# Optimization experiments

Measured on AMD Instinct MI355X. Metric: run time of the kernel, lower is better.

The kernel has to match this reference:

```python
import jax, jax.numpy as jnp
import numpy as np

NSTEP, NGRID, MU = 730, 2000, 16
PRECS = 1e-5

# HBV parameter scaling ranges (parascaLst)
_LO = np.array([1, 50, 0.05, 0.01, 0.001, 0.2, 0, 0, -2.5, 0.5, 0, 0, 0.3], dtype=np.float32)
_HI = np.array([6, 1000, 0.9, 0.5, 0.2, 1, 10, 100, 2.5, 10, 0.1, 0.2, 5], dtype=np.float32)


def setup_inputs() -> dict:
    key = jax.random.key(0)
    k1, k2 = jax.random.split(key)
    u = jax.random.uniform(k1, (NSTEP, NGRID, 3), dtype=jnp.float32)
    # channel 0: precip [0,10]; channel 1: temp [-5,15]; channel 2: PET [0,5]
    scale = jnp.array([10.0, 20.0, 5.0], dtype=jnp.float32)
    shift = jnp.array([0.0, -5.0, 0.0], dtype=jnp.float32)
    x = u * scale + shift
    parameters = jax.random.uniform(k2, (NGRID, 13, MU), dtype=jnp.float32)
    return {"x": x, "parameters": parameters, "mu": MU}


def _hbv_forward(x, parameters, mu):
    Ngrid = x.shape[1]
    lo = jnp.asarray(_LO)[None, :, None]
    hi = jnp.asarray(_HI)[None, :, None]
    p = lo + parameters * (hi - lo)  # [Ngrid, 13, mu]
    (parBETA, parFC, parK0, parK1, parK2, parLP, parPERC, parUZL,
     parTT, parCFMAX, parCFR, parCWH, parBETAET) = [p[:, i, :] for i in range(13)]

    init = jnp.full((Ngrid, mu), 0.001, dtype=jnp.float32)
    state0 = (init, init, init, init, init)  # SNOWPACK, MELTWATER, SM, SUZ, SLZ

    def step(carry, inp):
        SP, MW, SM, SUZ, SLZ = carry
        Pt, Tt, Et = inp  # each [Ngrid]
        Pt, Tt, Et = Pt[:, None], Tt[:, None], Et[:, None]  # broadcast over mu
        rain = Pt * (Tt >= parTT).astype(jnp.float32)
        snow = Pt * (Tt < parTT).astype(jnp.float32)
        SP = SP + snow
        melt = jnp.minimum(jnp.maximum(parCFMAX * (Tt - parTT), 0.0), SP)
        MW = MW + melt
        SP = SP - melt
        refreezing = jnp.minimum(jnp.maximum(parCFR * parCFMAX * (parTT - Tt), 0.0), MW)
        SP = SP + refreezing
        MW = MW - refreezing
        tosoil = jnp.maximum(MW - parCWH * SP, 0.0)
        MW = MW - tosoil
        soil_wetness = jnp.clip((SM / parFC) ** parBETA, 0.0, 1.0)
        recharge = (rain + tosoil) * soil_wetness
        SM = SM + rain + tosoil - recharge
        excess = jnp.maximum(SM - parFC, 0.0)
        SM = SM - excess
        evapfactor = jnp.clip((SM / (parLP * parFC)) ** parBETAET, 0.0, 1.0)
        ETact = jnp.minimum(SM, Et * evapfactor)
        SM = jnp.maximum(SM - ETact, PRECS)
        SUZ = SUZ + recharge + excess
        PERC = jnp.minimum(SUZ, parPERC)
        SUZ = SUZ - PERC
        Q0 = parK0 * jnp.maximum(SUZ - parUZL, 0.0)
        SUZ = SUZ - Q0
        Q1 = parK1 * SUZ
        SUZ = SUZ - Q1
        SLZ = SLZ + PERC
        Q2 = parK2 * SLZ
        SLZ = SLZ - Q2
        return (SP, MW, SM, SUZ, SLZ), Q0 + Q1 + Q2

    xs = (x[:, :, 0], x[:, :, 1], x[:, :, 2])
    _, Qsimmu = jax.lax.scan(step, state0, xs)  # [Nstep, Ngrid, mu]
    Qsimave = Qsimmu.mean(-1)  # muwts=None -> mean over components
    return Qsimave[..., None]  # [Nstep, Ngrid, 1]  (routOpt=False)


def reference(x, parameters, mu):
    return _hbv_forward(x, parameters, mu)
```

## Files before the change

### kernel.cpp

```cpp
#include <hip/hip_runtime.h>

#define NSTEP  730
#define NGRID  2000
#define PRECSf 1e-5f

#define GLOBAL_AS __attribute__((address_space(1)))
#define LDS_AS    __attribute__((address_space(3)))

__device__ __forceinline__ float fast_exp2(float v) { return __builtin_amdgcn_exp2f(v); }
__device__ __forceinline__ float fast_log2(float v) { return __builtin_amdgcn_logf(v); }
__device__ __forceinline__ float med3(float a, float b, float c) {
    return __builtin_amdgcn_fmed3f(a, b, c);
}

struct Par {
    float TT, cfmax, cfmaxTT, cfrXcf, cfrTT, CWH;
    float beta, betaC, FC, betaet, betaetC;
    float PERC, omK0, k0uzl, omK1, K2;
};

#define MEMFENCE() asm volatile("" ::: "memory")
#define WAITV(N)  asm volatile("s_waitcnt vmcnt(" #N ")" ::: "memory")

__device__ __forceinline__ float route_step(float infl,
        float& SUZ, float& SLZ, const Par& c)
{
    const float SUZ1  = SUZ + infl;
    const float PERCv = fminf(SUZ1, c.PERC);
    const float SUZ2  = SUZ1 - PERCv;
    const float SUZ3  = fminf(SUZ2, fmaf(c.omK0, SUZ2, c.k0uzl));
    const float SUZ4  = c.omK1 * SUZ3;
    SUZ = SUZ4;
    const float SLZ1 = SLZ + PERCv;
    const float Q2   = c.K2 * SLZ1;
    SLZ = SLZ1 - Q2;
    return (SUZ2 - SUZ4) + Q2;
}

template<int I, bool SNOW>
__device__ __forceinline__ void step1(const float4 (&xv)[16],
        const float (&A)[16], const float (&Ets)[16],
        float (&An)[16], float (&Etn)[16],
        float (&qbuf)[16], float& infl,
        float& SM, float& SUZ, float& SLZ,
        float& SP, float& MW, const Par& c)
{
    const float Ac   = A[I];
    const float Et   = Ets[I];
    const float SMpA = SM + Ac;
    const float lg   = fast_log2(SM);
    float rain = 0.0f, SP2v = 0.0f, MW1v = 0.0f, rrawv = 0.0f, Ex = 0.0f;
    if constexpr (SNOW) {
        const float Pt = xv[I].x, Tt = xv[I].y;
        Ex = xv[I].z;
        const float snow = (Tt < c.TT) ? Pt : 0.0f;
        rain = Pt - snow;
        const float mraw = fmaf(c.cfmax, Tt, -c.cfmaxTT);
        rrawv = fmaf(-c.cfrXcf, Tt, c.cfrTT);
        const float SP1 = SP + snow;
        SP2v = med3(SP1 - mraw, 0.0f, SP1);
        MW1v = MW + (SP1 - SP2v);
    }
    const float sw = fast_exp2(fmaf(c.beta, lg, c.betaC));
    if constexpr (I >= 1) qbuf[I - 1] = route_step(infl, SUZ, SLZ, c);
    const float SM1 = fmaf(-Ac, sw, SMpA);
    const float lg1 = fast_log2(SM1);
    if constexpr (SNOW) {
        const float MW2 = med3(MW1v - rrawv, 0.0f, MW1v);
        SP = SP2v + (MW1v - MW2);
        const float tosoil = fmaxf(fmaf(-c.CWH, SP, MW2), 0.0f);
        MW = MW2 - tosoil;
        An[I]  = rain + tosoil;
        Etn[I] = Ex;
    }
    const float SM2 = fminf(SM1, c.FC);
    infl = SMpA - SM2;
    const float Ete = Et * fast_exp2(fmaf(c.betaet, lg1, c.betaetC));
    SM = fmaxf(fmaxf(SM2 - Ete, SM2 - Et), PRECSf);
}

template<int I, int NS, bool SNOW>
__device__ __forceinline__ void steps_pass(const float4 (&xv)[16],
        const float (&A)[16], const float (&Ets)[16],
        float (&An)[16], float (&Etn)[16],
        float (&qbuf)[16], float& infl,
        float& SM, float& SUZ, float& SLZ,
        float& SP, float& MW, const Par& c)
{
    if constexpr (I < NS) {
        step1<I, SNOW>(xv, A, Ets, An, Etn, qbuf, infl, SM, SUZ, SLZ, SP, MW, c);
        steps_pass<I + 1, NS, SNOW>(xv, A, Ets, An, Etn, qbuf, infl,
                                    SM, SUZ, SLZ, SP, MW, c);
    }
}

template<int I, int NS>
__device__ __forceinline__ void snow_pass(const float4 (&xv)[16],
        float& SP, float& MW, float (&A)[16], float (&Ets)[16], const Par& c)
{
    if constexpr (I < NS) {
        const float Pt = xv[I].x, Tt = xv[I].y, Ex = xv[I].z;
        const float snow = (Tt < c.TT) ? Pt : 0.0f;
        const float rain = Pt - snow;
        const float mraw = fmaf(c.cfmax, Tt, -c.cfmaxTT);
        const float rraw = fmaf(-c.cfrXcf, Tt, c.cfrTT);
        const float SP1  = SP + snow;
        const float SP2  = med3(SP1 - mraw, 0.0f, SP1);
        const float MW1  = MW + (SP1 - SP2);
        const float MW2  = med3(MW1 - rraw, 0.0f, MW1);
        SP = SP2 + (MW1 - MW2);
        const float tosoil = fmaxf(fmaf(-c.CWH, SP, MW2), 0.0f);
        MW = MW2 - tosoil;
        A[I]   = rain + tosoil;
        Ets[I] = Ex;
        snow_pass<I + 1, NS>(xv, SP, MW, A, Ets, c);
    }
}

#define LOAD_XV(B)                                                             \
    _Pragma("unroll")                                                          \
    for (int ii = 0; ii < 16; ++ii)                                            \
        xv[ii] = *reinterpret_cast<const float4*>(&xs[B][ii * 16 + crow * 4]); \
    asm volatile("" :: "v"(xv[0].x),  "v"(xv[1].x),  "v"(xv[2].x),             \
                       "v"(xv[3].x),  "v"(xv[4].x),  "v"(xv[5].x),             \
                       "v"(xv[6].x),  "v"(xv[7].x),  "v"(xv[8].x),             \
                       "v"(xv[9].x),  "v"(xv[10].x), "v"(xv[11].x),            \
                       "v"(xv[12].x), "v"(xv[13].x), "v"(xv[14].x),            \
                       "v"(xv[15].x))

#define REDUCE_STORE(T0, N) do {                                               \
    float* qrow = &qt[crow * 336 + m * 20];                                    \
    *reinterpret_cast<float4*>(qrow + 0)  = make_float4(qbuf[0], qbuf[1], qbuf[2], qbuf[3]);    \
    *reinterpret_cast<float4*>(qrow + 4)  = make_float4(qbuf[4], qbuf[5], qbuf[6], qbuf[7]);    \
    *reinterpret_cast<float4*>(qrow + 8)  = make_float4(qbuf[8], qbuf[9], qbuf[10], qbuf[11]);  \
    *reinterpret_cast<float4*>(qrow + 12) = make_float4(qbuf[12], qbuf[13], qbuf[14], qbuf[15]);\
    const float* qcol = &qt[crow * 336 + m];                                   \
    float s0 = qcol[0*20]  + qcol[1*20];                                       \
    float s1 = qcol[2*20]  + qcol[3*20];                                       \
    float s2 = qcol[4*20]  + qcol[5*20];                                       \
    float s3 = qcol[6*20]  + qcol[7*20];                                       \
    float s4 = qcol[8*20]  + qcol[9*20];                                       \
    float s5 = qcol[10*20] + qcol[11*20];                                      \
    float s6 = qcol[12*20] + qcol[13*20];                                      \
    float s7 = qcol[14*20] + qcol[15*20];                                      \
    s0 += s1; s2 += s3; s4 += s5; s6 += s7;                                    \
    s0 += s2; s4 += s6; s0 += s4;                                              \
    if (m < (N)) out[(size_t)((T0) + m) * NGRID + g] = s0 * 0.0625f;           \
} while (0)

__global__ __launch_bounds__(64, 1)
void hbv_kernel(const float* __restrict__ x,
                const float* __restrict__ params,
                float* __restrict__ out)
{
    __shared__ __align__(16) float xs[2][256];
    __shared__ __align__(16) float qt[4 * 336];

    const int lane = threadIdx.x;
    const int g0   = blockIdx.x * 4;
    const int crow = lane >> 4;
    const int m    = lane & 15;
    const int g    = g0 + crow;

    const float* srcb[4];
    int ioff[4];
#pragma unroll
    for (int j = 0; j < 4; ++j) {
        const int flat = j * 64 + lane;
        const int i    = flat >> 4;
        const int cc   = (flat >> 2) & 3;
        int comp       = flat & 3; if (comp == 3) comp = 0;
        srcb[j] = x + (size_t)(g0 + cc) * 3 + comp;
        ioff[j] = i;
    }

#define ISSUE(B, T0) do {                                                      \
    MEMFENCE();                                                                \
    _Pragma("unroll")                                                          \
    for (int j = 0; j < 4; ++j) {                                              \
        int stp = (T0) + ioff[j]; stp = stp < NSTEP ? stp : NSTEP - 1;         \
        const float* s_ = srcb[j] + (size_t)stp * (NGRID * 3);                 \
        __builtin_amdgcn_global_load_lds((const GLOBAL_AS unsigned*)s_,        \
            (LDS_AS unsigned*)&xs[B][j * 64], 4, 0, 0);                        \
    }                                                                          \
    MEMFENCE();                                                                \
} while (0)

    const float lo[13] = {1.f,50.f,0.05f,0.01f,0.001f,0.2f,0.f,0.f,-2.5f,0.5f,0.f,0.f,0.3f};
    const float hi[13] = {6.f,1000.f,0.9f,0.5f,0.2f,1.f,10.f,100.f,2.5f,10.f,0.1f,0.2f,5.f};
    float p[13];
    const float* pg = params + ((size_t)g * 13) * 16 + m;
#pragma unroll
    for (int i = 0; i < 13; ++i) p[i] = lo[i] + pg[(size_t)i * 16] * (hi[i] - lo[i]);

    Par c;
    c.TT      = p[8];
    c.cfmax   = p[9];
    c.cfmaxTT = p[9] * p[8];
    c.cfrXcf  = p[10] * p[9];
    c.cfrTT   = c.cfrXcf * p[8];
    c.CWH     = p[11];
    c.beta    = p[0];
    c.betaC   = -p[0] * fast_log2(p[1]);
    c.FC      = p[1];
    c.betaet  = p[12];
    c.betaetC = -p[12] * fast_log2(p[5] * p[1]);
    c.PERC    = p[6];
    c.omK0    = 1.0f - p[2];
    c.k0uzl   = p[2] * p[7];
    c.omK1    = 1.0f - p[3];
    c.K2      = p[4];

    float SP = 0.001f, MW = 0.001f, SM = 0.001f, SUZ = 0.001f, SLZ = 0.001f;

    float4 xv[16];
    float Aa[16], Eta[16];
    float Ab[16], Etb[16];
    float qbuf[16];
    float infl = 0.0f;

    ISSUE(0, 0);
    ISSUE(1, 16);
    WAITV(4);
    LOAD_XV(0);
    snow_pass<0, 16>(xv, SP, MW, Aa, Eta, c);

#define BODY_W(K, WN, AC_, ETC_, AN_, ETN_)                                    \
    WAITV(WN);                                                                 \
    LOAD_XV(((K) + 1) & 1);                                                    \
    ISSUE((K) & 1, ((K) + 2) * 16);                                            \
    steps_pass<0, 16, true>(xv, AC_, ETC_, AN_, ETN_, qbuf, infl,              \
                            SM, SUZ, SLZ, SP, MW, c);                          \
    qbuf[15] = route_step(infl, SUZ, SLZ, c);                                  \
    REDUCE_STORE((K) * 16, 16);

    BODY_W(0, 0, Aa, Eta, Ab, Etb);

    for (int kk = 0; kk < 22; ++kk) {
        const int k0 = 1 + kk * 2;
        BODY_W(k0,     16, Ab, Etb, Aa, Eta);
        BODY_W(k0 + 1, 16, Aa, Eta, Ab, Etb);
    }
#undef BODY_W

    steps_pass<0, 10, false>(xv, Ab, Etb, Aa, Eta, qbuf, infl,
                             SM, SUZ, SLZ, SP, MW, c);
    qbuf[9] = route_step(infl, SUZ, SLZ, c);
    REDUCE_STORE(720, 10);
#undef ISSUE
}

extern "C" void kernel_launch(void* const* d_in, const int* in_sizes, int n_in,
                              void* d_out, int out_size, void* d_ws, size_t ws_size,
                              hipStream_t stream)
{
    const float* x      = (const float*)d_in[0];
    const float* params = (const float*)d_in[1];
    float* out          = (float*)d_out;

    hipLaunchKernelGGL(hbv_kernel, dim3(500), dim3(64), 0, stream, x, params, out);
}
```

Baseline: 80.15 us.

## Replace hardware log2/exp2 with polynomial approximations and fold Et into exponent

```diff
diff --git a/kernel.cpp b/kernel.cpp
--- a/kernel.cpp
+++ b/kernel.cpp
@@ -7,15 +7,45 @@
 #define GLOBAL_AS __attribute__((address_space(1)))
 #define LDS_AS    __attribute__((address_space(3)))
 
-__device__ __forceinline__ float fast_exp2(float v) { return __builtin_amdgcn_exp2f(v); }
 __device__ __forceinline__ float fast_log2(float v) { return __builtin_amdgcn_logf(v); }
 __device__ __forceinline__ float med3(float a, float b, float c) {
     return __builtin_amdgcn_fmed3f(a, b, c);
 }
 
+struct Lg { float L; float ef; };
+__device__ __forceinline__ Lg plog2(float x) {
+    const int   i  = __float_as_int(x);
+    const int   ea = (i - 0x3F3504F3) >> 23;
+    const float m  = __int_as_float(i - (ea << 23));
+    const float t  = m - 1.0f;
+    const float pA = fmaf(t, -0.5f,        1.0f);
+    const float pB = fmaf(t, -0.25f,       0.33333333f);
+    const float pC = fmaf(t, -0.16666667f, 0.2f);
+    const float t2 = t * t;
+    const float pC2 = fmaf(t2, 0.14285714f, pC);
+    const float pAB = fmaf(t2, pB, pA);
+    const float t4  = t2 * t2;
+    const float B   = fmaf(t4, pC2, pAB);
+    Lg r; r.L = t * B; r.ef = (float)ea;
+    return r;
+}
+
+__device__ __forceinline__ float pexp2(float y) {
+    const float z  = y + 12582912.0f;
+    const float kf = z - 12582912.0f;
+    const float f  = y - kf;
+    const float qA = fmaf(f, 0.69314718f,   1.0f);
+    const float qB = fmaf(f, 0.055504109f,  0.24022651f);
+    const float qC = fmaf(f, 0.0013333558f, 0.0096181291f);
+    const float f2 = f * f;
+    const float qBC = fmaf(f2, qC, qB);
+    const float p   = fmaf(f2, qBC, qA);
+    return ldexpf(p, (int)kf);
+}
+
 struct Par {
     float TT, cfmax, cfmaxTT, cfrXcf, cfrTT, CWH;
-    float beta, betaC, FC, betaet, betaetC;
+    float beta, betal, betaC, FC, betaet, betaetl, betaetC;
     float PERC, omK0, k0uzl, omK1, K2;
 };
 
@@ -39,16 +69,17 @@
 
 template<int I, bool SNOW>
 __device__ __forceinline__ void step1(const float4 (&xv)[16],
-        const float (&A)[16], const float (&Ets)[16],
-        float (&An)[16], float (&Etn)[16],
+        const float (&A)[16], const float (&Ets)[16], const float (&cEts)[16],
+        float (&An)[16], float (&Etn)[16], float (&cEtn)[16],
         float (&qbuf)[16], float& infl,
         float& SM, float& SUZ, float& SLZ,
         float& SP, float& MW, const Par& c)
 {
     const float Ac   = A[I];
     const float Et   = Ets[I];
+    const float cEt  = cEts[I];
     const float SMpA = SM + Ac;
-    const float lg   = fast_log2(SM);
+    const Lg l0 = plog2(SM);
     float rain = 0.0f, SP2v = 0.0f, MW1v = 0.0f, rrawv = 0.0f, Ex = 0.0f;
     if constexpr (SNOW) {
         const float Pt = xv[I].x, Tt = xv[I].y;
@@ -61,10 +92,11 @@
         SP2v = med3(SP1 - mraw, 0.0f, SP1);
         MW1v = MW + (SP1 - SP2v);
     }
-    const float sw = fast_exp2(fmaf(c.beta, lg, c.betaC));
+    const float arg0 = fmaf(c.betal, l0.L, fmaf(c.beta, l0.ef, c.betaC));
+    const float sw   = pexp2(arg0);
     if constexpr (I >= 1) qbuf[I - 1] = route_step(infl, SUZ, SLZ, c);
     const float SM1 = fmaf(-Ac, sw, SMpA);
-    const float lg1 = fast_log2(SM1);
+    const Lg l1 = plog2(SM1);
     if constexpr (SNOW) {
         const float MW2 = med3(MW1v - rrawv, 0.0f, MW1v);
         SP = SP2v + (MW1v - MW2);
@@ -72,31 +104,35 @@
         MW = MW2 - tosoil;
         An[I]  = rain + tosoil;
         Etn[I] = Ex;
+        cEtn[I] = c.betaetC + fmaxf(fast_log2(Ex), -150.0f);
     }
     const float SM2 = fminf(SM1, c.FC);
+    const float arg1 = fmaf(c.betaetl, l1.L, fmaf(c.betaet, l1.ef, cEt));
+    const float Ete  = pexp2(arg1);
     infl = SMpA - SM2;
-    const float Ete = Et * fast_exp2(fmaf(c.betaet, lg1, c.betaetC));
     SM = fmaxf(fmaxf(SM2 - Ete, SM2 - Et), PRECSf);
 }
 
 template<int I, int NS, bool SNOW>
 __device__ __forceinline__ void steps_pass(const float4 (&xv)[16],
-        const float (&A)[16], const float (&Ets)[16],
-        float (&An)[16], float (&Etn)[16],
+        const float (&A)[16], const float (&Ets)[16], const float (&cEts)[16],
+        float (&An)[16], float (&Etn)[16], float (&cEtn)[16],
         float (&qbuf)[16], float& infl,
         float& SM, float& SUZ, float& SLZ,
         float& SP, float& MW, const Par& c)
 {
     if constexpr (I < NS) {
-        step1<I, SNOW>(xv, A, Ets, An, Etn, qbuf, infl, SM, SUZ, SLZ, SP, MW, c);
-        steps_pass<I + 1, NS, SNOW>(xv, A, Ets, An, Etn, qbuf, infl,
+        step1<I, SNOW>(xv, A, Ets, cEts, An, Etn, cEtn, qbuf, infl,
+                       SM, SUZ, SLZ, SP, MW, c);
+        steps_pass<I + 1, NS, SNOW>(xv, A, Ets, cEts, An, Etn, cEtn, qbuf, infl,
                                     SM, SUZ, SLZ, SP, MW, c);
     }
 }
 
 template<int I, int NS>
 __device__ __forceinline__ void snow_pass(const float4 (&xv)[16],
-        float& SP, float& MW, float (&A)[16], float (&Ets)[16], const Par& c)
+        float& SP, float& MW, float (&A)[16], float (&Ets)[16], float (&cEts)[16],
+        const Par& c)
 {
     if constexpr (I < NS) {
         const float Pt = xv[I].x, Tt = xv[I].y, Ex = xv[I].z;
@@ -113,7 +149,8 @@
         MW = MW2 - tosoil;
         A[I]   = rain + tosoil;
         Ets[I] = Ex;
-        snow_pass<I + 1, NS>(xv, SP, MW, A, Ets, c);
+        cEts[I] = c.betaetC + fmaxf(fast_log2(Ex), -150.0f);
+        snow_pass<I + 1, NS>(xv, SP, MW, A, Ets, cEts, c);
     }
 }
 
@@ -201,9 +238,11 @@
     c.cfrTT   = c.cfrXcf * p[8];
     c.CWH     = p[11];
     c.beta    = p[0];
+    c.betal   = p[0] * 1.4426950408f;
     c.betaC   = -p[0] * fast_log2(p[1]);
     c.FC      = p[1];
     c.betaet  = p[12];
+    c.betaetl = p[12] * 1.4426950408f;
     c.betaetC = -p[12] * fast_log2(p[5] * p[1]);
     c.PERC    = p[6];
     c.omK0    = 1.0f - p[2];
@@ -214,8 +253,8 @@
     float SP = 0.001f, MW = 0.001f, SM = 0.001f, SUZ = 0.001f, SLZ = 0.001f;
 
     float4 xv[16];
-    float Aa[16], Eta[16];
-    float Ab[16], Etb[16];
+    float Aa[16], Eta[16], cEa[16];
+    float Ab[16], Etb[16], cEb[16];
     float qbuf[16];
     float infl = 0.0f;
 
@@ -223,27 +262,27 @@
     ISSUE(1, 16);
     WAITV(4);
     LOAD_XV(0);
-    snow_pass<0, 16>(xv, SP, MW, Aa, Eta, c);
-
-#define BODY_W(K, WN, AC_, ETC_, AN_, ETN_)                                    \
+    snow_pass<0, 16>(xv, SP, MW, Aa, Eta, cEa, c);
+
+#define BODY_W(K, WN, AC_, ETC_, CEC_, AN_, ETN_, CEN_)                        \
     WAITV(WN);                                                                 \
     LOAD_XV(((K) + 1) & 1);                                                    \
     ISSUE((K) & 1, ((K) + 2) * 16);                                            \
-    steps_pass<0, 16, true>(xv, AC_, ETC_, AN_, ETN_, qbuf, infl,              \
+    steps_pass<0, 16, true>(xv, AC_, ETC_, CEC_, AN_, ETN_, CEN_, qbuf, infl,  \
                             SM, SUZ, SLZ, SP, MW, c);                          \
     qbuf[15] = route_step(infl, SUZ, SLZ, c);                                  \
     REDUCE_STORE((K) * 16, 16);
 
-    BODY_W(0, 0, Aa, Eta, Ab, Etb);
+    BODY_W(0, 0, Aa, Eta, cEa, Ab, Etb, cEb);
 
     for (int kk = 0; kk < 22; ++kk) {
         const int k0 = 1 + kk * 2;
-        BODY_W(k0,     16, Ab, Etb, Aa, Eta);
-        BODY_W(k0 + 1, 16, Aa, Eta, Ab, Etb);
+        BODY_W(k0,     1, Ab, Etb, cEb, Aa, Eta, cEa);
+        BODY_W(k0 + 1, 1, Aa, Eta, cEa, Ab, Etb, cEb);
     }
 #undef BODY_W
 
-    steps_pass<0, 10, false>(xv, Ab, Etb, Aa, Eta, qbuf, infl,
+    steps_pass<0, 10, false>(xv, Ab, Etb, cEb, Aa, Eta, cEa, qbuf, infl,
                              SM, SUZ, SLZ, SP, MW, c);
     qbuf[9] = route_step(infl, SUZ, SLZ, c);
     REDUCE_STORE(720, 10);
```

New measurement: 140.9 us (median of 2 runs). 1.76x slower.
